# Kernel optimization log

Hardware: AMD Instinct MI355X
Metric: run time of the kernel (lower is better)

## Reference

```python
import jax, jax.numpy as jnp
import numpy as np

C = 64
C2 = C // 2

def setup_inputs() -> dict:
    key = jax.random.key(0)
    ks = jax.random.split(key, 5)
    x = jax.random.normal(ks[0], (8, C, 64, 64), dtype=jnp.float32)
    # 1x1 conv weights stored as [out, in] matrices (kernel size 1)
    g_w = jax.random.normal(ks[1], (C2, C), dtype=jnp.float32) * (1.0 / np.sqrt(C))
    g_b = jax.random.normal(ks[2], (C2,), dtype=jnp.float32) * 0.01
    W_w = jax.random.normal(ks[3], (C, C2), dtype=jnp.float32) * (1.0 / np.sqrt(C2))
    W_b = jax.random.normal(ks[4], (C,), dtype=jnp.float32) * 0.01
    return {"x": x, "g_w": g_w, "g_b": g_b, "W_w": W_w, "W_b": W_b}

def reference(x, g_w, g_b, W_w, W_b):
    b, c, h, w = x.shape
    xf = x.reshape(b, c, h * w)                      # [B, C, N]
    # g: 1x1 conv -> [B, N, C2]
    g_x = jnp.einsum('oc,bcn->bno', g_w, xf) + g_b
    # attention scores on raw x (theta/phi convs unused in original forward)
    f = jnp.einsum('bcn,bcm->bnm', xf, xf)           # [B, N, N]
    f_div_C = jax.nn.softmax(f, axis=-1)
    y = jnp.einsum('bnm,bmo->bno', f_div_C, g_x)     # [B, N, C2]
    # W: 1x1 conv back to C channels, then residual
    W_y = jnp.einsum('co,bno->bcn', W_w, y) + W_b[None, :, None]
    z = W_y.reshape(b, c, h, w) + x
    return z
```

## Files before the change

kernel.cpp:

```cpp
#include <hip/hip_runtime.h>
#include <hip/hip_bf16.h>

#define BATCH 8
#define CH    64
#define CH2   32
#define NN    4096
#define BN    (BATCH * NN)
#define KPAD  72
#define VPAD  72
#define YPAD  36
#define RPAD  40
#define MAXSPLIT 8

typedef __attribute__((ext_vector_type(8)))  short        short8;
typedef __attribute__((ext_vector_type(4)))  float        floatx4;
typedef __attribute__((ext_vector_type(16))) float        floatx16;
typedef __attribute__((ext_vector_type(4)))  unsigned int uint4v;
typedef __attribute__((ext_vector_type(8)))  unsigned short ushort8v;
typedef unsigned short ushort_t;

#define LOG2E      1.4426950408889634f
#define SQRT_LOG2E 1.2011224087864498f

__device__ __forceinline__ unsigned short f2bf_rne(float f) {
    unsigned int u = __float_as_uint(f);
    return (unsigned short)((u + 0x7FFFu + ((u >> 16) & 1u)) >> 16);
}

__global__ __launch_bounds__(256) void prep_fused(const float* __restrict__ x,
                                                  const float* __restrict__ gw,
                                                  const float* __restrict__ gb,
                                                  ushort_t* __restrict__ xT,
                                                  float* __restrict__ mlog,
                                                  ushort_t* __restrict__ gxT) {
    __shared__ float gwl[CH2 * CH];
    __shared__ float gbl[CH2];
    int t = threadIdx.x;
    for (int i = t; i < CH2 * CH; i += 256) gwl[i] = gw[i];
    if (t < CH2) gbl[t] = gb[t];
    __syncthreads();

    int g   = blockIdx.x * 256 + t;
    int row = g >> 2;
    int q4  = g & 3;
    int b = row >> 12, n = row & (NN - 1);
    const float* xp = x + (size_t)b * CH * NN + n;

    float xv[16];
    #pragma unroll
    for (int j = 0; j < 16; ++j) xv[j] = xp[(size_t)(q4 * 16 + j) * NN];

    float ns = 0.f;
    short8 v0, v1;
    #pragma unroll
    for (int j = 0; j < 8; ++j) {
        ns += xv[j] * xv[j];
        v0[j] = (short)f2bf_rne(xv[j] * SQRT_LOG2E);
    }
    #pragma unroll
    for (int j = 0; j < 8; ++j) {
        ns += xv[8 + j] * xv[8 + j];
        v1[j] = (short)f2bf_rne(xv[8 + j] * SQRT_LOG2E);
    }
    *(short8*)(xT + (size_t)row * CH + q4 * 16)     = v0;
    *(short8*)(xT + (size_t)row * CH + q4 * 16 + 8) = v1;
    ns += __shfl_xor(ns, 1);
    ns += __shfl_xor(ns, 2);
    if (q4 == 0) mlog[row] = 12.0f * sqrtf(ns) * LOG2E;

    float acc[CH2];
    #pragma unroll
    for (int o = 0; o < CH2; ++o) {
        const float4* wr = (const float4*)(gwl + o * CH + q4 * 16);
        float4 w0 = wr[0], w1 = wr[1], w2 = wr[2], w3 = wr[3];
        float a;
        a  = w0.x * xv[0]  + w0.y * xv[1]  + w0.z * xv[2]  + w0.w * xv[3];
        a += w1.x * xv[4]  + w1.y * xv[5]  + w1.z * xv[6]  + w1.w * xv[7];
        a += w2.x * xv[8]  + w2.y * xv[9]  + w2.z * xv[10] + w2.w * xv[11];
        a += w3.x * xv[12] + w3.y * xv[13] + w3.z * xv[14] + w3.w * xv[15];
        acc[o] = a;
    }
    #pragma unroll
    for (int o = 0; o < CH2; ++o) {
        acc[o] += __shfl_xor(acc[o], 1);
        acc[o] += __shfl_xor(acc[o], 2);
    }
    #pragma unroll
    for (int i = 0; i < 8; ++i) {
        int o = q4 * 8 + i;
        gxT[((size_t)b * CH2 + o) * NN + n] = f2bf_rne(acc[o] + gbl[o]);
    }
}

__global__ __launch_bounds__(256, 4) void flash_attn(const ushort_t* __restrict__ xT,
                                                     const ushort_t* __restrict__ gxT,
                                                     const float* __restrict__ mlog,
                                                     ushort_t* __restrict__ py,
                                                     float* __restrict__ pl,
                                                     int ksplit) {
    __shared__ __align__(16) unsigned char smem[18432];
    ushort_t* Klds = (ushort_t*)smem;
    ushort_t* Vlds = Klds + 64 * KPAD;

    const int tid = threadIdx.x, wave = tid >> 6, lane = tid & 63;
    const int q5 = lane & 31;
    const int h  = lane >> 5;
    const int bq = blockIdx.x & 255;
    const int sp = blockIdx.x >> 8;
    const int b = bq >> 5, qt = bq & 31;
    const int n0 = qt * 128 + wave * 32;
    const int k0 = sp * ksplit;

    short8 qf[4];
    {
        const ushort_t* qp = xT + ((size_t)(b * NN + n0 + q5)) * CH + h * 8;
        #pragma unroll
        for (int f = 0; f < 4; ++f) qf[f] = *(const short8*)(qp + f * 16);
    }
    const float ml = mlog[(size_t)b * NN + n0 + q5];

    floatx16 mlC;
    #pragma unroll
    for (int i = 0; i < 16; ++i) mlC[i] = -ml;

    floatx16 yt;
    #pragma unroll
    for (int i = 0; i < 16; ++i) yt[i] = 0.f;
    float lsum = 0.f;

    const ushort_t* kb = xT + (size_t)(b * NN + k0) * CH;
    const ushort_t* vb = gxT + (size_t)b * CH2 * NN + k0;
    const int iters = ksplit >> 6;
    const int skey = tid >> 3, sc0 = (tid & 7) * 8;

    for (int kt = 0; kt < iters; ++kt) {
        const size_t kof = (size_t)kt << 12;
        short8 gk0 = *(const short8*)(kb + kof + (size_t)skey * CH + sc0);
        short8 gk1 = *(const short8*)(kb + kof + (size_t)(skey + 32) * CH + sc0);
        short8 gv  = *(const short8*)(vb + (size_t)skey * NN + kt * 64 + sc0);

        __syncthreads();
        *(short8*)(&Klds[skey * KPAD + sc0])        = gk0;
        *(short8*)(&Klds[(skey + 32) * KPAD + sc0]) = gk1;
        *(short8*)(&Vlds[skey * VPAD + sc0])        = gv;
        __syncthreads();

        short8 vf[4];
        #pragma unroll
        for (int fr = 0; fr < 4; ++fr)
            vf[fr] = *(const short8*)(&Vlds[q5 * VPAD + fr * 16 + h * 8]);

        #pragma unroll
        for (int T = 0; T < 2; ++T) {
            floatx16 st;
            __builtin_amdgcn_s_setprio(1);
            {
                short8 kf = *(const short8*)(&Klds[(T * 32 + q5) * KPAD + h * 8]);
                st = __builtin_amdgcn_mfma_f32_32x32x16_bf16(kf, qf[0], mlC, 0, 0, 0);
            }
            #pragma unroll
            for (int f = 1; f < 4; ++f) {
                short8 kf = *(const short8*)(&Klds[(T * 32 + q5) * KPAD + f * 16 + h * 8]);
                st = __builtin_amdgcn_mfma_f32_32x32x16_bf16(kf, qf[f], st, 0, 0, 0);
            }
            __builtin_amdgcn_s_setprio(0);
            unsigned int d[8];
            #pragma unroll
            for (int r2 = 0; r2 < 8; ++r2) {
                float p0 = __builtin_amdgcn_exp2f(st[2 * r2]);
                float p1 = __builtin_amdgcn_exp2f(st[2 * r2 + 1]);
                lsum += p0;
                lsum += p1;
                unsigned int pk;
                asm("v_cvt_pk_bf16_f32 %0, %1, %2" : "=v"(pk) : "v"(p0), "v"(p1));
                d[r2] = pk;
            }
            #pragma unroll
            for (int fp = 0; fp < 2; ++fp) {
                unsigned int b0 = d[fp * 4 + 0], b1 = d[fp * 4 + 1];
                unsigned int b2 = d[fp * 4 + 2], b3 = d[fp * 4 + 3];
                asm("v_permlane32_swap_b32 %0, %1" : "+v"(b0), "+v"(b2));
                asm("v_permlane32_swap_b32 %0, %1" : "+v"(b1), "+v"(b3));
                uint4v bv;
                bv[0] = b0; bv[1] = b1; bv[2] = b2; bv[3] = b3;
                short8 pb = __builtin_bit_cast(short8, bv);
                __builtin_amdgcn_s_setprio(1);
                yt = __builtin_amdgcn_mfma_f32_32x32x16_bf16(vf[T * 2 + fp], pb, yt, 0, 0, 0);
                __builtin_amdgcn_s_setprio(0);
            }
        }
    }

    lsum += __shfl_xor(lsum, 32);

    __syncthreads();
    float* yb = (float*)smem + wave * 32 * YPAD;
    #pragma unroll
    for (int reg = 0; reg < 16; ++reg) {
        int o = (reg & 3) + 8 * (reg >> 2) + 4 * h;
        yb[q5 * YPAD + o] = yt[reg];
    }
    __syncthreads();
    {
        int qq = lane >> 1, half = lane & 1;
        const float* src = yb + qq * YPAD + half * 16;
        float4 s0 = *(const float4*)(src);
        float4 s1 = *(const float4*)(src + 4);
        float4 s2 = *(const float4*)(src + 8);
        float4 s3 = *(const float4*)(src + 12);
        ushort8v pk0, pk1;
        pk0[0] = f2bf_rne(s0.x); pk0[1] = f2bf_rne(s0.y);
        pk0[2] = f2bf_rne(s0.z); pk0[3] = f2bf_rne(s0.w);
        pk0[4] = f2bf_rne(s1.x); pk0[5] = f2bf_rne(s1.y);
        pk0[6] = f2bf_rne(s1.z); pk0[7] = f2bf_rne(s1.w);
        pk1[0] = f2bf_rne(s2.x); pk1[1] = f2bf_rne(s2.y);
        pk1[2] = f2bf_rne(s2.z); pk1[3] = f2bf_rne(s2.w);
        pk1[4] = f2bf_rne(s3.x); pk1[5] = f2bf_rne(s3.y);
        pk1[6] = f2bf_rne(s3.z); pk1[7] = f2bf_rne(s3.w);
        ushort_t* dst = py + ((size_t)sp * BN + (size_t)b * NN + n0 + qq) * CH2 + half * 16;
        *(ushort8v*)(dst)     = pk0;
        *(ushort8v*)(dst + 8) = pk1;
    }
    if (h == 0) pl[(size_t)sp * BN + (size_t)b * NN + n0 + q5] = lsum;
}

__global__ __launch_bounds__(256) void reduce_proj(const ushort_t* __restrict__ py,
                                                   const float* __restrict__ pl,
                                                   const float* __restrict__ Ww,
                                                   const float* __restrict__ Wb,
                                                   const float* __restrict__ x,
                                                   float* __restrict__ out,
                                                   int nsplit) {
    __shared__ ushort_t WwB[CH * RPAD];
    __shared__ ushort_t Y[64 * RPAD];
    __shared__ float    linv[64];
    __shared__ float    WbL[CH];

    const int t = threadIdx.x;
    const int row = t >> 2, o8 = (t & 3) * 8;
    const int grow0 = blockIdx.x * 64;

    {
        const float* wp = Ww + row * CH2 + o8;
        ushort8v w;
        #pragma unroll
        for (int j = 0; j < 8; ++j) w[j] = f2bf_rne(wp[j]);
        *(ushort8v*)(&WwB[row * RPAD + o8]) = w;
    }
    if (t < CH) WbL[t] = Wb[t];
    if (t < 64) {
        const float* plp = pl + grow0 + t;
        float lv[MAXSPLIT];
        #pragma unroll
        for (int s = 0; s < MAXSPLIT; ++s) {
            int sc = s < nsplit ? s : 0;
            lv[s] = plp[(size_t)sc * BN];
        }
        float l = 0.f;
        #pragma unroll
        for (int s = 0; s < MAXSPLIT; ++s) if (s < nsplit) l += lv[s];
        linv[t] = 1.0f / l;
    }

    float acc[8];
    #pragma unroll
    for (int j = 0; j < 8; ++j) acc[j] = 0.f;
    {
        const ushort_t* pp = py + ((size_t)(grow0 + row)) * CH2 + o8;
        ushort8v pv[MAXSPLIT];
        #pragma unroll
        for (int s = 0; s < MAXSPLIT; ++s) {
            int sc = s < nsplit ? s : 0;
            pv[s] = *(const ushort8v*)(pp + (size_t)sc * BN * CH2);
        }
        #pragma unroll
        for (int s = 0; s < MAXSPLIT; ++s) if (s < nsplit) {
            #pragma unroll
            for (int j = 0; j < 8; ++j)
                acc[j] += __uint_as_float((unsigned int)pv[s][j] << 16);
        }
    }
    __syncthreads();
    {
        float inv = linv[row];
        ushort8v yv;
        #pragma unroll
        for (int j = 0; j < 8; ++j) yv[j] = f2bf_rne(acc[j] * inv);
        *(ushort8v*)(&Y[row * RPAD + o8]) = yv;
    }
    __syncthreads();

    const int wave = t >> 6, lane = t & 63;
    const int ql = lane & 15, quad = lane >> 4;
    const int b = grow0 >> 12;
    const int nbase = (grow0 & (NN - 1)) + wave * 16;

    short8 bfrag = *(const short8*)(&Y[(wave * 16 + ql) * RPAD + quad * 8]);
    #pragma unroll
    for (int ct = 0; ct < 4; ++ct) {
        short8 afrag = *(const short8*)(&WwB[(ct * 16 + ql) * RPAD + quad * 8]);
        floatx4 d = (floatx4){0.f, 0.f, 0.f, 0.f};
        d = __builtin_amdgcn_mfma_f32_16x16x32_bf16(afrag, bfrag, d, 0, 0, 0);
        #pragma unroll
        for (int r = 0; r < 4; ++r) {
            int c = ct * 16 + quad * 4 + r;
            size_t oi = ((size_t)b * CH + c) * NN + nbase + ql;
            out[oi] = d[r] + WbL[c] + x[oi];
        }
    }
}

extern "C" void kernel_launch(void* const* d_in, const int* in_sizes, int n_in,
                              void* d_out, int out_size, void* d_ws, size_t ws_size,
                              hipStream_t stream) {
    const float* x  = (const float*)d_in[0];
    const float* gw = (const float*)d_in[1];
    const float* gb = (const float*)d_in[2];
    const float* Ww = (const float*)d_in[3];
    const float* Wb = (const float*)d_in[4];
    float* out = (float*)d_out;

    ushort_t* xT   = (ushort_t*)d_ws;
    ushort_t* gxT  = xT + (size_t)BN * CH;
    float*    mlog = (float*)(gxT + (size_t)BATCH * CH2 * NN);
    ushort_t* py   = (ushort_t*)(mlog + BN);
    size_t base_bytes = (size_t)BN * CH * 2 + (size_t)BATCH * CH2 * NN * 2 + (size_t)BN * 4;
    int split = MAXSPLIT;
    while (split > 1 && base_bytes + (size_t)split * BN * (CH2 * 2 + 4) > ws_size)
        split >>= 1;
    float* pl = (float*)(py + (size_t)split * BN * CH2);

    hipLaunchKernelGGL(prep_fused,  dim3(BN * 4 / 256), dim3(256), 0, stream,
                       x, gw, gb, xT, mlog, gxT);
    hipLaunchKernelGGL(flash_attn,  dim3(256 * split),  dim3(256), 0, stream,
                       xT, gxT, mlog, py, pl, NN / split);
    hipLaunchKernelGGL(reduce_proj, dim3(BN / 64),      dim3(256), 0, stream,
                       py, pl, Ww, Wb, x, out, split);
}
```

Before: 112.0 us.

## Stage x through LDS in prep, widen attention key tile, double reduce threads

The prep kernel now loads a 32-column tile of x into padded shared memory with coalesced reads, then has 8 threads per row compute the bf16 transpose, the norm and the g projection. The flash attention kernel processes 128 keys per iteration instead of 64, which halves the number of barrier pairs, and it loads V fragments from LDS right before each MFMA. The reduce/projection kernel moves to 512 threads so each wave computes two output channel tiles. In exchange, attention uses more LDS per block, which may lower occupancy, and the extra shuffles in prep add some cost.

```diff
diff --git a/kernel.cpp b/kernel.cpp
--- a/kernel.cpp
+++ b/kernel.cpp
@@ -7,7 +7,7 @@
 #define NN    4096
 #define BN    (BATCH * NN)
 #define KPAD  72
-#define VPAD  72
+#define VPAD  136
 #define YPAD  36
 #define RPAD  40
 #define MAXSPLIT 8
@@ -17,6 +17,7 @@
 typedef __attribute__((ext_vector_type(16))) float        floatx16;
 typedef __attribute__((ext_vector_type(4)))  unsigned int uint4v;
 typedef __attribute__((ext_vector_type(8)))  unsigned short ushort8v;
+typedef __attribute__((ext_vector_type(4)))  unsigned short ushort4v;
 typedef unsigned short ushort_t;
 
 #define LOG2E      1.4426950408889634f
@@ -35,59 +36,62 @@
                                                   ushort_t* __restrict__ gxT) {
     __shared__ float gwl[CH2 * CH];
     __shared__ float gbl[CH2];
-    int t = threadIdx.x;
+    __shared__ float xl[CH][33];
+
+    const int t = threadIdx.x;
     for (int i = t; i < CH2 * CH; i += 256) gwl[i] = gw[i];
     if (t < CH2) gbl[t] = gb[t];
-    __syncthreads();
-
-    int g   = blockIdx.x * 256 + t;
-    int row = g >> 2;
-    int q4  = g & 3;
-    int b = row >> 12, n = row & (NN - 1);
-    const float* xp = x + (size_t)b * CH * NN + n;
-
-    float xv[16];
-    #pragma unroll
-    for (int j = 0; j < 16; ++j) xv[j] = xp[(size_t)(q4 * 16 + j) * NN];
+
+    const int b  = blockIdx.x >> 7;
+    const int n0 = (blockIdx.x & 127) * 32;
+
+    {
+        const int nl = t & 31, cg = (t >> 5) * 8;
+        const float* xpp = x + ((size_t)b * CH + cg) * NN + n0 + nl;
+        #pragma unroll
+        for (int j = 0; j < 8; ++j) xl[cg + j][nl] = xpp[(size_t)j * NN];
+    }
+    __syncthreads();
+
+    const int row = t >> 3;
+    const int o8  = t & 7;
+    const int n   = n0 + row;
+    const int growg = b * NN + n;
+
+    float xv[8];
+    #pragma unroll
+    for (int j = 0; j < 8; ++j) xv[j] = xl[o8 * 8 + j][row];
 
     float ns = 0.f;
-    short8 v0, v1;
+    short8 v0;
     #pragma unroll
     for (int j = 0; j < 8; ++j) {
         ns += xv[j] * xv[j];
         v0[j] = (short)f2bf_rne(xv[j] * SQRT_LOG2E);
     }
-    #pragma unroll
-    for (int j = 0; j < 8; ++j) {
-        ns += xv[8 + j] * xv[8 + j];
-        v1[j] = (short)f2bf_rne(xv[8 + j] * SQRT_LOG2E);
-    }
-    *(short8*)(xT + (size_t)row * CH + q4 * 16)     = v0;
-    *(short8*)(xT + (size_t)row * CH + q4 * 16 + 8) = v1;
+    *(short8*)(xT + (size_t)growg * CH + o8 * 8) = v0;
     ns += __shfl_xor(ns, 1);
     ns += __shfl_xor(ns, 2);
-    if (q4 == 0) mlog[row] = 12.0f * sqrtf(ns) * LOG2E;
+    ns += __shfl_xor(ns, 4);
+    if (o8 == 0) mlog[growg] = 12.0f * sqrtf(ns) * LOG2E;
 
     float acc[CH2];
     #pragma unroll
     for (int o = 0; o < CH2; ++o) {
-        const float4* wr = (const float4*)(gwl + o * CH + q4 * 16);
-        float4 w0 = wr[0], w1 = wr[1], w2 = wr[2], w3 = wr[3];
-        float a;
-        a  = w0.x * xv[0]  + w0.y * xv[1]  + w0.z * xv[2]  + w0.w * xv[3];
-        a += w1.x * xv[4]  + w1.y * xv[5]  + w1.z * xv[6]  + w1.w * xv[7];
-        a += w2.x * xv[8]  + w2.y * xv[9]  + w2.z * xv[10] + w2.w * xv[11];
-        a += w3.x * xv[12] + w3.y * xv[13] + w3.z * xv[14] + w3.w * xv[15];
-        acc[o] = a;
+        const float4* wr = (const float4*)(gwl + o * CH + o8 * 8);
+        float4 w0 = wr[0], w1 = wr[1];
+        acc[o] = w0.x * xv[0] + w0.y * xv[1] + w0.z * xv[2] + w0.w * xv[3]
+               + w1.x * xv[4] + w1.y * xv[5] + w1.z * xv[6] + w1.w * xv[7];
     }
     #pragma unroll
     for (int o = 0; o < CH2; ++o) {
         acc[o] += __shfl_xor(acc[o], 1);
         acc[o] += __shfl_xor(acc[o], 2);
-    }
-    #pragma unroll
-    for (int i = 0; i < 8; ++i) {
-        int o = q4 * 8 + i;
+        acc[o] += __shfl_xor(acc[o], 4);
+    }
+    #pragma unroll
+    for (int i = 0; i < 4; ++i) {
+        int o = o8 * 4 + i;
         gxT[((size_t)b * CH2 + o) * NN + n] = f2bf_rne(acc[o] + gbl[o]);
     }
 }
@@ -98,9 +102,9 @@
                                                      ushort_t* __restrict__ py,
                                                      float* __restrict__ pl,
                                                      int ksplit) {
-    __shared__ __align__(16) unsigned char smem[18432];
+    __shared__ __align__(16) unsigned char smem[(128 * KPAD + 32 * VPAD) * 2];
     ushort_t* Klds = (ushort_t*)smem;
-    ushort_t* Vlds = Klds + 64 * KPAD;
+    ushort_t* Vlds = Klds + 128 * KPAD;
 
     const int tid = threadIdx.x, wave = tid >> 6, lane = tid & 63;
     const int q5 = lane & 31;
@@ -130,28 +134,30 @@
 
     const ushort_t* kb = xT + (size_t)(b * NN + k0) * CH;
     const ushort_t* vb = gxT + (size_t)b * CH2 * NN + k0;
-    const int iters = ksplit >> 6;
+    const int iters = ksplit >> 7;
     const int skey = tid >> 3, sc0 = (tid & 7) * 8;
+    const int vc0 = (tid & 7) * 16;
 
     for (int kt = 0; kt < iters; ++kt) {
-        const size_t kof = (size_t)kt << 12;
-        short8 gk0 = *(const short8*)(kb + kof + (size_t)skey * CH + sc0);
+        const size_t kof = (size_t)kt << 13;
+        short8 gk0 = *(const short8*)(kb + kof + (size_t)(skey     ) * CH + sc0);
         short8 gk1 = *(const short8*)(kb + kof + (size_t)(skey + 32) * CH + sc0);
-        short8 gv  = *(const short8*)(vb + (size_t)skey * NN + kt * 64 + sc0);
+        short8 gk2 = *(const short8*)(kb + kof + (size_t)(skey + 64) * CH + sc0);
+        short8 gk3 = *(const short8*)(kb + kof + (size_t)(skey + 96) * CH + sc0);
+        short8 gv0 = *(const short8*)(vb + (size_t)skey * NN + kt * 128 + vc0);
+        short8 gv1 = *(const short8*)(vb + (size_t)skey * NN + kt * 128 + vc0 + 8);
 
         __syncthreads();
-        *(short8*)(&Klds[skey * KPAD + sc0])        = gk0;
+        *(short8*)(&Klds[(skey     ) * KPAD + sc0]) = gk0;
         *(short8*)(&Klds[(skey + 32) * KPAD + sc0]) = gk1;
-        *(short8*)(&Vlds[skey * VPAD + sc0])        = gv;
+        *(short8*)(&Klds[(skey + 64) * KPAD + sc0]) = gk2;
+        *(short8*)(&Klds[(skey + 96) * KPAD + sc0]) = gk3;
+        *(short8*)(&Vlds[skey * VPAD + vc0])     = gv0;
+        *(short8*)(&Vlds[skey * VPAD + vc0 + 8]) = gv1;
         __syncthreads();
 
-        short8 vf[4];
-        #pragma unroll
-        for (int fr = 0; fr < 4; ++fr)
-            vf[fr] = *(const short8*)(&Vlds[q5 * VPAD + fr * 16 + h * 8]);
-
-        #pragma unroll
-        for (int T = 0; T < 2; ++T) {
+        #pragma unroll
+        for (int T = 0; T < 4; ++T) {
             floatx16 st;
             __builtin_amdgcn_s_setprio(1);
             {
@@ -184,8 +190,9 @@
                 uint4v bv;
                 bv[0] = b0; bv[1] = b1; bv[2] = b2; bv[3] = b3;
                 short8 pb = __builtin_bit_cast(short8, bv);
+                short8 vf = *(const short8*)(&Vlds[q5 * VPAD + T * 32 + fp * 16 + h * 8]);
                 __builtin_amdgcn_s_setprio(1);
-                yt = __builtin_amdgcn_mfma_f32_32x32x16_bf16(vf[T * 2 + fp], pb, yt, 0, 0, 0);
+                yt = __builtin_amdgcn_mfma_f32_32x32x16_bf16(vf, pb, yt, 0, 0, 0);
                 __builtin_amdgcn_s_setprio(0);
             }
         }
@@ -224,7 +231,7 @@
     if (h == 0) pl[(size_t)sp * BN + (size_t)b * NN + n0 + q5] = lsum;
 }
 
-__global__ __launch_bounds__(256) void reduce_proj(const ushort_t* __restrict__ py,
+__global__ __launch_bounds__(512) void reduce_proj(const ushort_t* __restrict__ py,
                                                    const float* __restrict__ pl,
                                                    const float* __restrict__ Ww,
                                                    const float* __restrict__ Wb,
@@ -237,15 +244,15 @@
     __shared__ float    WbL[CH];
 
     const int t = threadIdx.x;
-    const int row = t >> 2, o8 = (t & 3) * 8;
     const int grow0 = blockIdx.x * 64;
 
-    {
-        const float* wp = Ww + row * CH2 + o8;
+    if (t < 256) {
+        const int r = t >> 2, o8 = (t & 3) * 8;
+        const float* wp = Ww + r * CH2 + o8;
         ushort8v w;
         #pragma unroll
         for (int j = 0; j < 8; ++j) w[j] = f2bf_rne(wp[j]);
-        *(ushort8v*)(&WwB[row * RPAD + o8]) = w;
+        *(ushort8v*)(&WwB[r * RPAD + o8]) = w;
     }
     if (t < CH) WbL[t] = Wb[t];
     if (t < 64) {
@@ -262,42 +269,44 @@
         linv[t] = 1.0f / l;
     }
 
-    float acc[8];
-    #pragma unroll
-    for (int j = 0; j < 8; ++j) acc[j] = 0.f;
-    {
-        const ushort_t* pp = py + ((size_t)(grow0 + row)) * CH2 + o8;
-        ushort8v pv[MAXSPLIT];
+    const int row = t >> 3, o4 = (t & 7) * 4;
+    float acc[4] = {0.f, 0.f, 0.f, 0.f};
+    {
+        const ushort_t* pp = py + (size_t)(grow0 + row) * CH2 + o4;
+        ushort4v pv[MAXSPLIT];
         #pragma unroll
         for (int s = 0; s < MAXSPLIT; ++s) {
             int sc = s < nsplit ? s : 0;
-            pv[s] = *(const ushort8v*)(pp + (size_t)sc * BN * CH2);
+            pv[s] = *(const ushort4v*)(pp + (size_t)sc * BN * CH2);
         }
         #pragma unroll
         for (int s = 0; s < MAXSPLIT; ++s) if (s < nsplit) {
             #pragma unroll
-            for (int j = 0; j < 8; ++j)
+            for (int j = 0; j < 4; ++j)
                 acc[j] += __uint_as_float((unsigned int)pv[s][j] << 16);
         }
     }
     __syncthreads();
     {
         float inv = linv[row];
-        ushort8v yv;
-        #pragma unroll
-        for (int j = 0; j < 8; ++j) yv[j] = f2bf_rne(acc[j] * inv);
-        *(ushort8v*)(&Y[row * RPAD + o8]) = yv;
+        ushort4v yv;
+        #pragma unroll
+        for (int j = 0; j < 4; ++j) yv[j] = f2bf_rne(acc[j] * inv);
+        *(ushort4v*)(&Y[row * RPAD + o4]) = yv;
     }
     __syncthreads();
 
     const int wave = t >> 6, lane = t & 63;
     const int ql = lane & 15, quad = lane >> 4;
+    const int nt = wave & 3;
+    const int ctb = (wave >> 2) * 2;
     const int b = grow0 >> 12;
-    const int nbase = (grow0 & (NN - 1)) + wave * 16;
-
-    short8 bfrag = *(const short8*)(&Y[(wave * 16 + ql) * RPAD + quad * 8]);
-    #pragma unroll
-    for (int ct = 0; ct < 4; ++ct) {
+    const int nbase = (grow0 & (NN - 1)) + nt * 16;
+
+    short8 bfrag = *(const short8*)(&Y[(nt * 16 + ql) * RPAD + quad * 8]);
+    #pragma unroll
+    for (int ci = 0; ci < 2; ++ci) {
+        int ct = ctb + ci;
         short8 afrag = *(const short8*)(&WwB[(ct * 16 + ql) * RPAD + quad * 8]);
         floatx4 d = (floatx4){0.f, 0.f, 0.f, 0.f};
         d = __builtin_amdgcn_mfma_f32_16x16x32_bf16(afrag, bfrag, d, 0, 0, 0);
@@ -330,10 +339,10 @@
         split >>= 1;
     float* pl = (float*)(py + (size_t)split * BN * CH2);
 
-    hipLaunchKernelGGL(prep_fused,  dim3(BN * 4 / 256), dim3(256), 0, stream,
+    hipLaunchKernelGGL(prep_fused,  dim3(BN / 32),     dim3(256), 0, stream,
                        x, gw, gb, xT, mlog, gxT);
-    hipLaunchKernelGGL(flash_attn,  dim3(256 * split),  dim3(256), 0, stream,
+    hipLaunchKernelGGL(flash_attn,  dim3(256 * split), dim3(256), 0, stream,
                        xT, gxT, mlog, py, pl, NN / split);
-    hipLaunchKernelGGL(reduce_proj, dim3(BN / 64),      dim3(256), 0, stream,
+    hipLaunchKernelGGL(reduce_proj, dim3(BN / 64),     dim3(512), 0, stream,
                        py, pl, Ww, Wb, x, out, split);
 }
```

Result: slower. 117.6 us (+5.0%).
